# Kernel optimization log

Measured on AMD Instinct MI355X. Metric: run time of the kernel, lower is better.

Reference implementation:

```python
import jax, jax.numpy as jnp
import numpy as np
import math

D_MODEL = 1024
RANK = 128
K_RANK = 128
N_KNOW = 32768
COARSE_K = 64
FINE_K = 16
B, S = 2, 2048


def setup_inputs() -> dict:
    key = jax.random.key(0)
    ks = jax.random.split(key, 6)
    x = jax.random.normal(ks[0], (B, S, D_MODEL), dtype=jnp.float32)
    h = jax.random.normal(ks[1], (B, S, RANK), dtype=jnp.float32)
    W_router = jax.random.normal(ks[2], (D_MODEL, N_KNOW), dtype=jnp.float32) * 0.02
    W_q = jax.random.normal(ks[3], (K_RANK, RANK), dtype=jnp.float32) * 0.02  # Linear(rank->k_rank) weight
    K_all = jax.random.normal(ks[4], (N_KNOW, K_RANK), dtype=jnp.float32) * 0.02
    V_all = jax.random.normal(ks[5], (N_KNOW, D_MODEL), dtype=jnp.float32) * 0.02
    return {"x": x, "h": h, "W_router": W_router, "W_q": W_q, "K_all": K_all, "V_all": V_all}


def reference(x, h, W_router, W_q, K_all, V_all):
    # Stage 1: coarse candidate selection via router logits
    k_logits = jnp.einsum('bsd,dn->bsn', x, W_router)              # [B,S,N]
    coarse_scores, candidate_idx = jax.lax.top_k(k_logits, COARSE_K)  # [B,S,Ck]

    # Stage 2: fine matching with compressed query
    query = jnp.einsum('bsr,kr->bsk', h, W_q)                      # [B,S,K_RANK]
    K_cand = K_all[candidate_idx]                                  # [B,S,Ck,K_RANK] gather
    fine_scores = jnp.einsum('bsd,bscd->bsc', query, K_cand) / math.sqrt(K_RANK)
    fine_topk_scores, fine_local_idx = jax.lax.top_k(fine_scores, FINE_K)  # [B,S,Fk]
    fine_weights = jax.nn.softmax(fine_topk_scores, axis=-1)
    fine_global_idx = jnp.take_along_axis(candidate_idx, fine_local_idx, axis=-1)  # [B,S,Fk]

    selected_V = V_all[fine_global_idx]                            # [B,S,Fk,D] gather
    output = jnp.einsum('bsfd,bsf->bsd', selected_V, fine_weights)  # weighted combine
    return output
```

## Files before the change

kernel.cpp:

```cpp
#include <hip/hip_runtime.h>
#include <cstdint>

#define D_MODEL 1024
#define RANK 128
#define K_RANK_ 128
#define N_KNOW 32768
#define COARSE_K 64
#define FINE_K 16
#define NTOK 4096
#define MSEL 96
#define DELTA 1.0e-3f
#define SC 4096

using u32 = unsigned int;
using u64 = unsigned long long;
typedef _Float16 half8 __attribute__((ext_vector_type(8)));
typedef __attribute__((ext_vector_type(4))) float f32x4;

__device__ __forceinline__ u32 ordf(float v) {
    u32 u = __float_as_uint(v);
    return (u & 0x80000000u) ? ~u : (u | 0x80000000u);
}
__device__ __forceinline__ float unordf(u32 o) {
    return (o & 0x80000000u) ? __uint_as_float(o ^ 0x80000000u)
                             : __uint_as_float(~o);
}
__device__ __forceinline__ ushort f2h(float f) {
    union { _Float16 h; ushort u; } cv; cv.h = (_Float16)f; return cv.u;
}
__device__ __forceinline__ void gload16(const void* g, void* l) {
    __builtin_amdgcn_global_load_lds(
        (const __attribute__((address_space(1))) char*)g,
        (__attribute__((address_space(3))) char*)l, 16, 0, 0);
}

__global__ __launch_bounds__(256)
void kcvt_x(const float* __restrict__ in, ushort* __restrict__ xh)
{
    int i = blockIdx.x * 256 + threadIdx.x;
    float4 v = ((const float4*)in)[i];
    ((ushort4*)xh)[i] = make_ushort4(f2h(v.x), f2h(v.y), f2h(v.z), f2h(v.w));
}

__global__ __launch_bounds__(256)
void kcvt_wt(const float* __restrict__ W, ushort* __restrict__ out, int col0)
{
    __shared__ float tile[32][33];
    const int nb = blockIdx.x * 32;
    const int kb = blockIdx.y * 32;
    const int tx = threadIdx.x & 31, ty = threadIdx.x >> 5;
#pragma unroll
    for (int q = 0; q < 4; ++q)
        tile[ty + q * 8][tx] = W[(size_t)(kb + ty + q * 8) * N_KNOW + col0 + nb + tx];
    __syncthreads();
#pragma unroll
    for (int q = 0; q < 4; ++q) {
        float v = tile[tx][ty + q * 8];
        out[(size_t)(nb + ty + q * 8) * D_MODEL + kb + tx] = f2h(v);
    }
}

__global__ __launch_bounds__(512, 2)
void k1f8(const ushort* __restrict__ xh, const ushort* __restrict__ wt,
          float* __restrict__ L)
{
    __shared__ ushort lds[2][32768];

    const int tid = threadIdx.x;
    const int nwg = gridDim.x;
    int wfl = blockIdx.x;
    wfl = (wfl & 7) * (nwg >> 3) + (wfl >> 3);
    const int bm = (wfl & 15) * 256;
    const int bn = (wfl >> 4) * 256;

    const int lane = tid & 63;
    const int wid = tid >> 6;
    const int wm = wid >> 2, wn = wid & 3;
    const int lr = lane & 15, g = lane >> 4;

    const ushort* gA[4]; const ushort* gB[4];
#pragma unroll
    for (int i = 0; i < 4; ++i) {
        const int o = i * 512 + tid;
        const int row = o >> 3;
        const int gslot = (o & 7) ^ (row & 7);
        gA[i] = xh + (size_t)(bm + row) * D_MODEL + gslot * 8;
        gB[i] = wt + (size_t)(bn + row) * D_MODEL + gslot * 8;
    }

    int aoff[2][8], boff[2][4];
#pragma unroll
    for (int ks = 0; ks < 2; ++ks) {
#pragma unroll
        for (int mf = 0; mf < 8; ++mf) {
            int row = wm * 128 + mf * 16 + lr;
            aoff[ks][mf] = row * 128 + (((ks * 4 + g) ^ (row & 7)) << 4);
        }
#pragma unroll
        for (int nf = 0; nf < 4; ++nf) {
            int row = wn * 64 + nf * 16 + lr;
            boff[ks][nf] = 32768 + row * 128 + (((ks * 4 + g) ^ (row & 7)) << 4);
        }
    }

    f32x4 acc[8][4];
#pragma unroll
    for (int mf = 0; mf < 8; ++mf)
#pragma unroll
        for (int nf = 0; nf < 4; ++nf) acc[mf][nf] = (f32x4)(0.f);

#define STAGE(buf, kt)                                                         \
    {                                                                          \
        const int kadd = (kt) * 64;                                            \
        _Pragma("unroll")                                                      \
        for (int i = 0; i < 4; ++i) {                                          \
            gload16(gA[i] + kadd, (char*)&lds[(buf)][0] + (i * 512 + tid) * 16);\
            gload16(gB[i] + kadd,                                              \
                    (char*)&lds[(buf)][0] + 32768 + (i * 512 + tid) * 16);     \
        }                                                                      \
    }

    STAGE(0, 0);
    STAGE(1, 1);

    const int NKT = D_MODEL / 64;
    for (int kt = 0; kt < NKT; ++kt) {
        if (kt < NKT - 1) asm volatile("s_waitcnt vmcnt(8)" ::: "memory");
        else              asm volatile("s_waitcnt vmcnt(0)" ::: "memory");
        __builtin_amdgcn_s_barrier();
        asm volatile("" ::: "memory");

        const char* lb = (const char*)&lds[kt & 1][0];
#pragma unroll
        for (int ks = 0; ks < 2; ++ks) {
            half8 a[8], b[4];
#pragma unroll
            for (int mf = 0; mf < 8; ++mf)
                a[mf] = *(const half8*)(lb + aoff[ks][mf]);
#pragma unroll
            for (int nf = 0; nf < 4; ++nf)
                b[nf] = *(const half8*)(lb + boff[ks][nf]);
            __builtin_amdgcn_s_setprio(1);
#pragma unroll
            for (int mf = 0; mf < 8; ++mf)
#pragma unroll
                for (int nf = 0; nf < 4; ++nf)
                    acc[mf][nf] = __builtin_amdgcn_mfma_f32_16x16x32_f16(
                        a[mf], b[nf], acc[mf][nf], 0, 0, 0);
            __builtin_amdgcn_s_setprio(0);
        }

        asm volatile("" ::: "memory");
        __builtin_amdgcn_s_barrier();
        asm volatile("" ::: "memory");
        if (kt + 2 < NKT) STAGE(kt & 1, kt + 2);
    }
#undef STAGE

    const int crow0 = bm + wm * 128 + g * 4;
    const int ccol  = bn + wn * 64 + lr;
#pragma unroll
    for (int mf = 0; mf < 8; ++mf)
#pragma unroll
        for (int nf = 0; nf < 4; ++nf)
#pragma unroll
            for (int r = 0; r < 4; ++r)
                L[(size_t)(crow0 + mf * 16 + r) * SC + ccol + nf * 16] = acc[mf][nf][r];
}

template <int M>
__global__ __launch_bounds__(256)
void k2_topk(const float* __restrict__ L, u64* __restrict__ R,
             int col0, int stripe)
{
    const int tt = blockIdx.x;
    const int tid = threadIdx.x;

    __shared__ u64 buf[4224];
    __shared__ int scnt;
    __shared__ int sred[4];

    u64 key[16];
    const float4* row4 = (const float4*)(L + (size_t)tt * SC);
#pragma unroll
    for (int q = 0; q < 4; ++q) {
        float4 v = row4[q * 256 + tid];
        int c = col0 + (q * 256 + tid) * 4;
        key[q * 4 + 0] = ((u64)ordf(v.x) << 32) | (u32)(N_KNOW - 1 - c);
        key[q * 4 + 1] = ((u64)ordf(v.y) << 32) | (u32)(N_KNOW - 2 - c);
        key[q * 4 + 2] = ((u64)ordf(v.z) << 32) | (u32)(N_KNOW - 3 - c);
        key[q * 4 + 3] = ((u64)ordf(v.w) << 32) | (u32)(N_KNOW - 4 - c);
    }

    u64 tkey;
    if (stripe == 0) {
        u32 lo = 0, hi = 0xFFFFFFFFu;
        for (int it = 0; it < 28; ++it) {
            if (hi - lo <= 1) break;
            u32 mid = lo + ((hi - lo) >> 1);
            int c = 0;
#pragma unroll
            for (int j = 0; j < 16; ++j) c += ((u32)(key[j] >> 32) > mid) ? 1 : 0;
#pragma unroll
            for (int o = 32; o; o >>= 1) c += __shfl_xor(c, o);
            if ((tid & 63) == 0) sred[tid >> 6] = c;
            __syncthreads();
            c = sred[0] + sred[1] + sred[2] + sred[3];
            __syncthreads();
            if (c >= M) { lo = mid; if (c <= 768) break; }
            else hi = mid;
        }
        tkey = ((u64)lo << 32) | 0xFFFFFFFFull;
        if (tid == 0) scnt = 0;
    } else {
        tkey = R[(size_t)tt * M + (M - 1)];
        if (tid < M) buf[tid] = R[(size_t)tt * M + tid];
        if (tid == 0) scnt = M;
    }
    __syncthreads();

#pragma unroll
    for (int j = 0; j < 16; ++j)
        if (key[j] > tkey) {
            int p = atomicAdd(&scnt, 1);
            if (p < 4224) buf[p] = key[j];
        }
    __syncthreads();

    const int n = min(scnt, 4224);
    for (int i = tid; i < n; i += 256) {
        u64 ki = buf[i];
        int r = 0;
        for (int j = 0; j < n; ++j) r += (buf[j] > ki) ? 1 : 0;
        if (r < M) R[(size_t)tt * M + r] = ki;
    }
}

__global__ __launch_bounds__(256)
void k2b_band(const u64* __restrict__ R96, u32* __restrict__ jobs,
              int* __restrict__ jobCount, u32* __restrict__ band)
{
    __shared__ float sv[4][MSEL];
    const int tid = threadIdx.x;
    const int w = tid >> 6, lane = tid & 63;
    const int tt = blockIdx.x * 4 + w;

    sv[w][lane] = unordf((u32)(R96[(size_t)tt * MSEL + lane] >> 32));
    if (lane < MSEL - 64)
        sv[w][lane + 64] = unordf((u32)(R96[(size_t)tt * MSEL + lane + 64] >> 32));
    __syncthreads();

    const float t = sv[w][COARSE_K - 1];
    int cg = 0, cl = 0;
    for (int j = lane; j < MSEL; j += 64) {
        cg += (sv[w][j] > t + DELTA) ? 1 : 0;
        cl += (sv[w][j] < t - DELTA) ? 1 : 0;
    }
#pragma unroll
    for (int o = 32; o; o >>= 1) { cg += __shfl_xor(cg, o); cl += __shfl_xor(cl, o); }

    int lo = cg, hi = MSEL - 1 - cl;
    if (lo > COARSE_K - 1) lo = COARSE_K - 1;
    if (hi < COARSE_K - 1) hi = COARSE_K - 1;

    u32 b;
    if (lo == COARSE_K - 1 && hi == COARSE_K - 1) {
        b = 0x80000000u | 63u | (63u << 8);
    } else {
        int nj = hi - lo + 1;
        int base = 0;
        if (lane == 0) base = atomicAdd(jobCount, nj);
        base = __shfl(base, 0);
        for (int k = lane; k < nj; k += 64)
            jobs[base + k] = ((u32)tt << 8) | (u32)(lo + k);
        b = (u32)lo | ((u32)hi << 8);
    }
    if (lane == 0) band[tt] = b;
}

__global__ __launch_bounds__(256)
void k2b_exec(const u32* __restrict__ jobs, const int* __restrict__ jobCount,
              const u64* __restrict__ R96, const float* __restrict__ x,
              const float* __restrict__ W, u64* __restrict__ nk)
{
    __shared__ float red[4];
    const int tid = threadIdx.x;
    const int n = *jobCount;
    for (int j = blockIdx.x; j < n; j += gridDim.x) {
        u32 jd = jobs[j];
        int tt = jd >> 8, idx = jd & 255;
        u64 key = R96[(size_t)tt * MSEL + idx];
        int col = (N_KNOW - 1) - (int)(u32)(key & 0xFFFFFFFFu);
        float p = 0.f;
#pragma unroll
        for (int q = 0; q < 4; ++q) {
            int k = tid + q * 256;
            p = fmaf(x[(size_t)tt * D_MODEL + k], W[(size_t)k * N_KNOW + col], p);
        }
#pragma unroll
        for (int o = 32; o; o >>= 1) p += __shfl_xor(p, o);
        if ((tid & 63) == 0) red[tid >> 6] = p;
        __syncthreads();
        if (tid == 0) {
            float e = red[0] + red[1] + red[2] + red[3];
            nk[(size_t)tt * MSEL + idx] = ((u64)ordf(e) << 32) | (key & 0xFFFFFFFFu);
        }
        __syncthreads();
    }
}

__global__ __launch_bounds__(128)
void k2b_final(const u64* __restrict__ R96, const u64* __restrict__ nk,
               const u32* __restrict__ band, u64* __restrict__ R64)
{
    const int tt = blockIdx.x;
    const int tid = threadIdx.x;
    __shared__ u64 keys[MSEL];
    __shared__ u64 nkk[MSEL];

    const u32 b = band[tt];
    if (tid < MSEL) keys[tid] = R96[(size_t)tt * MSEL + tid];
    const int lo = b & 0xFF, hi = (b >> 8) & 0xFF;
    const bool trivial = (b & 0x80000000u) != 0;
    if (!trivial && tid >= lo && tid <= hi && tid < MSEL)
        nkk[tid] = nk[(size_t)tt * MSEL + tid];
    __syncthreads();

    if (trivial) {
        if (tid < COARSE_K) R64[(size_t)tt * COARSE_K + tid] = keys[tid];
        return;
    }
    if (tid < lo) R64[(size_t)tt * COARSE_K + tid] = keys[tid];
    const int mwin = COARSE_K - lo;
    if (tid >= lo && tid <= hi) {
        u64 me = nkk[tid];
        int r = 0;
        for (int j = lo; j <= hi; ++j) r += (nkk[j] > me) ? 1 : 0;
        if (r < mwin) R64[(size_t)tt * COARSE_K + lo + r] = keys[tid];
    }
}

__device__ __forceinline__ void fma4(float4& a, float w, const float4& v) {
    a.x = fmaf(w, v.x, a.x); a.y = fmaf(w, v.y, a.y);
    a.z = fmaf(w, v.z, a.z); a.w = fmaf(w, v.w, a.w);
}

__global__ __launch_bounds__(256)
void k3f(const float* __restrict__ h, const float* __restrict__ Wq,
         const float* __restrict__ Kall, const u64* __restrict__ R,
         int* __restrict__ fidx, float* __restrict__ fw)
{
    __shared__ float hq[4][RANK];
    __shared__ float qv[4][K_RANK_];

    const int tid = threadIdx.x;
    const int w = tid >> 6, lane = tid & 63;
    const int tt = blockIdx.x * 4 + w;

    {
        float2 hv = *(const float2*)(h + (size_t)tt * RANK + lane * 2);
        hq[w][lane * 2] = hv.x;
        hq[w][lane * 2 + 1] = hv.y;
    }
    const u64 key = R[(size_t)tt * COARSE_K + lane];
    const int ci = (N_KNOW - 1) - (int)(u32)(key & 0xFFFFFFFFu);
    __syncthreads();

    {
        float s0 = 0.f, s1 = 0.f;
        const float4* w0 = (const float4*)(Wq + (size_t)(lane * 2) * RANK);
        const float4* w1 = (const float4*)(Wq + (size_t)(lane * 2 + 1) * RANK);
#pragma unroll
        for (int r4 = 0; r4 < RANK / 4; ++r4) {
            float4 a = w0[r4], b = w1[r4];
            const float* hh = &hq[w][r4 * 4];
            s0 = fmaf(a.x, hh[0], s0); s0 = fmaf(a.y, hh[1], s0);
            s0 = fmaf(a.z, hh[2], s0); s0 = fmaf(a.w, hh[3], s0);
            s1 = fmaf(b.x, hh[0], s1); s1 = fmaf(b.y, hh[1], s1);
            s1 = fmaf(b.z, hh[2], s1); s1 = fmaf(b.w, hh[3], s1);
        }
        qv[w][lane * 2] = s0;
        qv[w][lane * 2 + 1] = s1;
    }
    __syncthreads();

    float sc;
    {
        float s = 0.f;
        const float4* kr = (const float4*)(Kall + (size_t)ci * K_RANK_);
#pragma unroll
        for (int r4 = 0; r4 < K_RANK_ / 4; ++r4) {
            float4 a = kr[r4];
            const float* qq = &qv[w][r4 * 4];
            s = fmaf(a.x, qq[0], s); s = fmaf(a.y, qq[1], s);
            s = fmaf(a.z, qq[2], s); s = fmaf(a.w, qq[3], s);
        }
        sc = s * 0.08838834764831845f;
    }

    const u64 myk = ((u64)ordf(sc) << 32) | (u32)(63 - lane);
    int rnk = 0;
#pragma unroll
    for (int j = 0; j < 64; ++j) {
        u64 kj = __shfl(myk, j);
        rnk += (kj > myk) ? 1 : 0;
    }

    float smax = sc;
#pragma unroll
    for (int o = 32; o; o >>= 1) smax = fmaxf(smax, __shfl_xor(smax, o));
    float e = (rnk < FINE_K) ? expf(sc - smax) : 0.f;
    float esum = e;
#pragma unroll
    for (int o = 32; o; o >>= 1) esum += __shfl_xor(esum, o);
    if (rnk < FINE_K) {
        fidx[(size_t)tt * FINE_K + rnk] = ci;
        fw[(size_t)tt * FINE_K + rnk] = e / esum;
    }
}

__global__ __launch_bounds__(256)
void k3g(const int* __restrict__ fidx, const float* __restrict__ fw,
         const float* __restrict__ Vall, float* __restrict__ out)
{
    __shared__ int si[FINE_K];
    __shared__ float sw[FINE_K];
    const int tt = blockIdx.x;
    const int tid = threadIdx.x;
    if (tid < FINE_K) {
        si[tid] = fidx[(size_t)tt * FINE_K + tid];
        sw[tid] = fw[(size_t)tt * FINE_K + tid];
    }
    __syncthreads();

    float4 a = make_float4(0.f, 0.f, 0.f, 0.f);
#pragma unroll
    for (int f = 0; f < FINE_K; ++f) {
        const float4 v = *(const float4*)(Vall + (size_t)si[f] * D_MODEL + tid * 4);
        fma4(a, sw[f], v);
    }
    ((float4*)(out + (size_t)tt * D_MODEL))[tid] = a;
}

extern "C" void kernel_launch(void* const* d_in, const int* in_sizes, int n_in,
                              void* d_out, int out_size, void* d_ws, size_t ws_size,
                              hipStream_t stream)
{
    const float* x  = (const float*)d_in[0];
    const float* h  = (const float*)d_in[1];
    const float* Wr = (const float*)d_in[2];
    const float* Wq = (const float*)d_in[3];
    const float* Ka = (const float*)d_in[4];
    const float* Va = (const float*)d_in[5];
    float* out = (float*)d_out;

    const size_t fixed =
        (size_t)NTOK * D_MODEL * 2 +
        (size_t)NTOK * SC * 4 +
        (size_t)NTOK * MSEL * 8 * 2 +
        (size_t)NTOK * COARSE_K * 8 +
        (size_t)NTOK * MSEL * 4 +
        4096 +
        (size_t)NTOK * 4 +
        (size_t)NTOK * FINE_K * 8;

    int WCH = N_KNOW;
    while (WCH > SC && fixed + (size_t)WCH * D_MODEL * 2 > ws_size)
        WCH >>= 1;

    char* p = (char*)d_ws;
    ushort* wt   = (ushort*)p;  p += (size_t)WCH * D_MODEL * 2;
    ushort* xh   = (ushort*)p;  p += (size_t)NTOK * D_MODEL * 2;
    float*  L    = (float*)p;   p += (size_t)NTOK * SC * 4;
    u64*    R96  = (u64*)p;     p += (size_t)NTOK * MSEL * 8;
    u64*    nk   = (u64*)p;     p += (size_t)NTOK * MSEL * 8;
    u64*    R64  = (u64*)p;     p += (size_t)NTOK * COARSE_K * 8;
    u32*    jobs = (u32*)p;     p += (size_t)NTOK * MSEL * 4;
    int*    jobCount = (int*)p; p += 4096;
    u32*    band = (u32*)p;     p += (size_t)NTOK * 4;
    int*    fidx = (int*)p;     p += (size_t)NTOK * FINE_K * 4;
    float*  fw   = (float*)p;   p += (size_t)NTOK * FINE_K * 4;

    hipMemsetAsync(jobCount, 0, 4, stream);

    kcvt_x<<<NTOK * D_MODEL / 4 / 256, 256, 0, stream>>>(x, xh);

    const int nstripe = N_KNOW / SC;
    const int spc = WCH / SC;
    for (int s = 0; s < nstripe; ++s) {
        if (s % spc == 0)
            kcvt_wt<<<dim3(WCH / 32, D_MODEL / 32), 256, 0, stream>>>(Wr, wt, s * SC);
        const ushort* wts = wt + (size_t)((s % spc) * SC) * D_MODEL;
        k1f8<<<(SC / 256) * (NTOK / 256), 512, 0, stream>>>(xh, wts, L);
        k2_topk<MSEL><<<NTOK, 256, 0, stream>>>(L, R96, s * SC, s);
    }

    k2b_band<<<NTOK / 4, 256, 0, stream>>>(R96, jobs, jobCount, band);
    k2b_exec<<<8192, 256, 0, stream>>>(jobs, jobCount, R96, x, Wr, nk);
    k2b_final<<<NTOK, 128, 0, stream>>>(R96, nk, band, R64);

    k3f<<<NTOK / 4, 256, 0, stream>>>(h, Wq, Ka, R64, fidx, fw);
    k3g<<<NTOK, 256, 0, stream>>>(fidx, fw, Va, out);
}
```

Baseline: 836.5 us.

## Interleave half-tile global loads with MFMA phases in router GEMM mainloop

Restructures the double-buffered router GEMM mainloop into finer phases. Each K tile is split into half-tile A and B global-to-LDS loads, issued between groups of 16 MFMAs, with separate waits and barriers per phase. The aim is to hide load latency and shorten barrier stalls by spreading memory traffic across the compute. The extra barriers and the tighter vmcnt accounting add synchronisation overhead and ordering risk.

```diff
diff --git a/kernel.cpp b/kernel.cpp
--- a/kernel.cpp
+++ b/kernel.cpp
@@ -109,53 +109,109 @@
 #pragma unroll
         for (int nf = 0; nf < 4; ++nf) acc[mf][nf] = (f32x4)(0.f);
 
-#define STAGE(buf, kt)                                                         \
+#define SAH(b, t, h)                                                           \
     {                                                                          \
-        const int kadd = (kt) * 64;                                            \
-        _Pragma("unroll")                                                      \
-        for (int i = 0; i < 4; ++i) {                                          \
-            gload16(gA[i] + kadd, (char*)&lds[(buf)][0] + (i * 512 + tid) * 16);\
-            gload16(gB[i] + kadd,                                              \
-                    (char*)&lds[(buf)][0] + 32768 + (i * 512 + tid) * 16);     \
-        }                                                                      \
-    }
-
-    STAGE(0, 0);
-    STAGE(1, 1);
-
-    const int NKT = D_MODEL / 64;
-    for (int kt = 0; kt < NKT; ++kt) {
-        if (kt < NKT - 1) asm volatile("s_waitcnt vmcnt(8)" ::: "memory");
-        else              asm volatile("s_waitcnt vmcnt(0)" ::: "memory");
-        __builtin_amdgcn_s_barrier();
-        asm volatile("" ::: "memory");
-
-        const char* lb = (const char*)&lds[kt & 1][0];
-#pragma unroll
-        for (int ks = 0; ks < 2; ++ks) {
-            half8 a[8], b[4];
-#pragma unroll
-            for (int mf = 0; mf < 8; ++mf)
-                a[mf] = *(const half8*)(lb + aoff[ks][mf]);
-#pragma unroll
-            for (int nf = 0; nf < 4; ++nf)
-                b[nf] = *(const half8*)(lb + boff[ks][nf]);
-            __builtin_amdgcn_s_setprio(1);
-#pragma unroll
-            for (int mf = 0; mf < 8; ++mf)
-#pragma unroll
-                for (int nf = 0; nf < 4; ++nf)
-                    acc[mf][nf] = __builtin_amdgcn_mfma_f32_16x16x32_f16(
-                        a[mf], b[nf], acc[mf][nf], 0, 0, 0);
-            __builtin_amdgcn_s_setprio(0);
-        }
-
-        asm volatile("" ::: "memory");
-        __builtin_amdgcn_s_barrier();
-        asm volatile("" ::: "memory");
-        if (kt + 2 < NKT) STAGE(kt & 1, kt + 2);
-    }
-#undef STAGE
+        gload16(gA[2*(h)]   + (t) * 64,                                        \
+                (char*)&lds[(b)][0] + ((2*(h)) * 512 + tid) * 16);             \
+        gload16(gA[2*(h)+1] + (t) * 64,                                        \
+                (char*)&lds[(b)][0] + ((2*(h)+1) * 512 + tid) * 16);           \
+    }
+#define SBH(b, t, h)                                                           \
+    {                                                                          \
+        gload16(gB[2*(h)]   + (t) * 64,                                        \
+                (char*)&lds[(b)][0] + 32768 + ((2*(h)) * 512 + tid) * 16);     \
+        gload16(gB[2*(h)+1] + (t) * 64,                                        \
+                (char*)&lds[(b)][0] + 32768 + ((2*(h)+1) * 512 + tid) * 16);   \
+    }
+
+#define LDA4(lb, ks, base)                                                     \
+    a0 = *(const half8*)((lb) + aoff[ks][(base) + 0]);                         \
+    a1 = *(const half8*)((lb) + aoff[ks][(base) + 1]);                         \
+    a2 = *(const half8*)((lb) + aoff[ks][(base) + 2]);                         \
+    a3 = *(const half8*)((lb) + aoff[ks][(base) + 3]);
+
+#define LDB4(lb, ks, bb)                                                       \
+    bb[0] = *(const half8*)((lb) + boff[ks][0]);                               \
+    bb[1] = *(const half8*)((lb) + boff[ks][1]);                               \
+    bb[2] = *(const half8*)((lb) + boff[ks][2]);                               \
+    bb[3] = *(const half8*)((lb) + boff[ks][3]);
+
+#define MFMA16(mbase, bb)                                                      \
+    __builtin_amdgcn_s_setprio(1);                                             \
+    _Pragma("unroll")                                                          \
+    for (int nf = 0; nf < 4; ++nf) {                                           \
+        acc[(mbase)+0][nf] = __builtin_amdgcn_mfma_f32_16x16x32_f16(           \
+            a0, bb[nf], acc[(mbase)+0][nf], 0, 0, 0);                          \
+        acc[(mbase)+1][nf] = __builtin_amdgcn_mfma_f32_16x16x32_f16(           \
+            a1, bb[nf], acc[(mbase)+1][nf], 0, 0, 0);                          \
+        acc[(mbase)+2][nf] = __builtin_amdgcn_mfma_f32_16x16x32_f16(           \
+            a2, bb[nf], acc[(mbase)+2][nf], 0, 0, 0);                          \
+        acc[(mbase)+3][nf] = __builtin_amdgcn_mfma_f32_16x16x32_f16(           \
+            a3, bb[nf], acc[(mbase)+3][nf], 0, 0, 0);                          \
+    }                                                                          \
+    __builtin_amdgcn_s_setprio(0);
+
+#define SBAR()                                                                 \
+    __builtin_amdgcn_sched_barrier(0);                                         \
+    __builtin_amdgcn_s_barrier();                                              \
+    __builtin_amdgcn_sched_barrier(0);
+
+    SBH(0, 0, 0); SBH(0, 0, 1);
+    SAH(0, 0, 0); SAH(0, 0, 1);
+    SBH(1, 1, 0); SBH(1, 1, 1);
+
+    const char* lb0 = (const char*)&lds[0][0];
+    const char* lb1 = (const char*)&lds[1][0];
+    half8 b0q[4], b1q[4];
+
+    for (int i = 0; i < 8; ++i) {
+        const int t1 = 2 * i + 1;
+        const int tn0 = 2 * i + 2, tn1 = 2 * i + 3;
+        const bool st = tn0 < 16;
+        half8 a0, a1, a2, a3;
+
+        asm volatile("s_waitcnt vmcnt(4)" ::: "memory");
+        SBAR();
+        LDA4(lb0, 0, 0);
+        LDB4(lb0, 0, b0q);
+        SAH(1, t1, 0);
+        MFMA16(0, b0q);
+        LDA4(lb0, 1, 0);
+        LDB4(lb0, 1, b1q);
+        SAH(1, t1, 1);
+        MFMA16(0, b1q);
+        SBAR();
+        LDA4(lb0, 0, 4);
+        if (st) SBH(0, tn0, 0);
+        MFMA16(4, b0q);
+        LDA4(lb0, 1, 4);
+        if (st) SBH(0, tn0, 1);
+        MFMA16(4, b1q);
+        if (i < 7) asm volatile("s_waitcnt vmcnt(4)" ::: "memory");
+        else       asm volatile("s_waitcnt vmcnt(0)" ::: "memory");
+        SBAR();
+        LDA4(lb1, 0, 0);
+        LDB4(lb1, 0, b0q);
+        if (st) SAH(0, tn0, 0);
+        MFMA16(0, b0q);
+        LDA4(lb1, 1, 0);
+        LDB4(lb1, 1, b1q);
+        if (st) SAH(0, tn0, 1);
+        MFMA16(0, b1q);
+        SBAR();
+        LDA4(lb1, 0, 4);
+        if (st) SBH(1, tn1, 0);
+        MFMA16(4, b0q);
+        LDA4(lb1, 1, 4);
+        if (st) SBH(1, tn1, 1);
+        MFMA16(4, b1q);
+    }
+#undef SAH
+#undef SBH
+#undef LDA4
+#undef LDB4
+#undef MFMA16
+#undef SBAR
 
     const int crow0 = bm + wm * 128 + g * 4;
     const int ccol  = bn + wn * 64 + lr;
```

Measured after the change: 821.6 us. Within noise of the previous version (-1.8%).
